# Kernel tuning notes

Measured on AMD Instinct MI355X. Metric: run time of the kernel, lower is better.

## Reference

```python
import jax, jax.numpy as jnp
import numpy as np


def _diag(x, ax1, ax2):
    """Extract diagonal over (ax1, ax2), placing the diag index back at ax1."""
    return jnp.moveaxis(jnp.diagonal(x, axis1=ax1, axis2=ax2), -1, ax1)


def _contractions(x):
    """All mean contractions of a 3rd-order equivariant tensor x: [B,n,n,n,C].
    Returns (a2 [B,n,n,6C], a1 [B,n,10C], a0 [B,5C])."""
    s1 = jnp.mean(x, axis=1)          # [B,n,n,C]
    s2 = jnp.mean(x, axis=2)
    s3 = jnp.mean(x, axis=3)
    d12 = _diag(x, 1, 2)              # x[b,i,i,k,c] -> [B,n,n,C]
    d13 = _diag(x, 1, 3)              # x[b,i,j,i,c]
    d23 = _diag(x, 2, 3)              # x[b,k,i,i,c]
    a2 = jnp.concatenate([s1, s2, s3, d12, d13, d23], axis=-1)  # [B,n,n,6C]

    # first-order: 3 double sums + 6 diag sums + 1 triple diag = 10C
    fo_double = [jnp.mean(x, axis=(1, 2)), jnp.mean(x, axis=(1, 3)),
                 jnp.mean(x, axis=(2, 3))]
    fo_diag = []
    for d in (d12, d13, d23):
        fo_diag.append(jnp.mean(d, axis=1))
        fo_diag.append(jnp.mean(d, axis=2))
    triple_diag = _diag(d23, 1, 2)    # x[b,i,i,i,c] -> [B,n,C]
    a1 = jnp.concatenate(fo_double + fo_diag + [triple_diag], axis=-1)  # [B,n,10C]

    # zeroth-order: triple sum + 3 diag double sums + triple-diag sum = 5C
    z = [jnp.mean(fo_double[0], axis=1)]
    z += [jnp.mean(d, axis=(1, 2)) for d in (d12, d13, d23)]
    z += [jnp.mean(triple_diag, axis=1)]
    a0 = jnp.concatenate(z, axis=-1)  # [B,5C]
    return a2, a1, a0


def _forward(x, W22, b22, W12, b12, W12t, b12t, W02, b02, W11, b11, W01, b01):
    a2, a1, a0 = _contractions(x)
    a2_w_t = jnp.concatenate([a2, jnp.swapaxes(a2, 1, 2)], axis=-1)  # [B,n,n,12C]
    # second-order mix -> [B,n,n,O]
    so = (a2_w_t @ W22 + b22
          + (a1 @ W12 + b12)[:, :, None, :]
          + (a1 @ W12t + b12t)[:, None, :, :]
          + (a0 @ W02 + b02)[:, None, None, :])
    # first-order mix -> [B,n,O], added onto the diagonal
    fo = a1 @ W11 + b11 + (a0 @ W01 + b01)[:, None, :]
    idx = jnp.arange(so.shape[1])
    return so.at[:, idx, idx, :].add(fo)


def setup_inputs() -> dict:
    key = jax.random.key(0)
    B, n, C, O = 8, 64, 32, 32
    ks = jax.random.split(key, 13)

    def w(k, fan_in):
        return (jax.random.normal(k, (fan_in, O), jnp.float32)
                / np.float32(np.sqrt(fan_in)))

    def b(k):
        return jax.random.normal(k, (O,), jnp.float32) * 0.02

    return {
        "x": jax.random.normal(ks[0], (B, n, n, n, C), jnp.float32),
        "W22": w(ks[1], 12 * C), "b22": b(ks[2]),
        "W12": w(ks[3], 10 * C), "b12": b(ks[4]),
        "W12t": w(ks[5], 10 * C), "b12t": b(ks[6]),
        "W02": w(ks[7], 5 * C), "b02": b(ks[8]),
        "W11": w(ks[9], 10 * C), "b11": b(ks[10]),
        "W01": w(ks[11], 5 * C), "b01": b(ks[12]),
    }


def reference(x, W22, b22, W12, b12, W12t, b12t, W02, b02, W11, b11, W01, b01):
    return _forward(x, W22, b22, W12, b12, W12t, b12t, W02, b02, W11, b11, W01, b01)
```

## Files before the change

kernel.cpp:

```cpp
#include <hip/hip_runtime.h>
#include <hip/hip_bf16.h>
#include <stdint.h>

#define NC   2048
#define NNC  131072
#define N3C  8388608
#define CMPE 1048576

typedef unsigned short u16;

__device__ __forceinline__ u16 bf16b(float x){
    unsigned u = __float_as_uint(x);
    u += 0x7FFFu + ((u >> 16) & 1u);
    return (u16)(u >> 16);
}
__device__ __forceinline__ float b2f(u16 h){ return __uint_as_float(((unsigned)h) << 16); }
__device__ __forceinline__ float lo16(unsigned u){ return __uint_as_float(u << 16); }
__device__ __forceinline__ float hi16(unsigned u){ return __uint_as_float(u & 0xFFFF0000u); }
__device__ __forceinline__ void f4acc(float4& a, const float4 b){
    a.x += b.x; a.y += b.y; a.z += b.z; a.w += b.w;
}
__device__ __forceinline__ void addp4(float4& a, const uint2 u){
    a.x += lo16(u.x); a.y += hi16(u.x); a.z += lo16(u.y); a.w += hi16(u.y);
}
__device__ __forceinline__ uint2 pack4(float4 v){
    uint2 r;
    r.x = (unsigned)bf16b(v.x) | ((unsigned)bf16b(v.y) << 16);
    r.y = (unsigned)bf16b(v.z) | ((unsigned)bf16b(v.w) << 16);
    return r;
}
__device__ __forceinline__ uint2 pack4s(float4 v, float s){
    v.x *= s; v.y *= s; v.z *= s; v.w *= s;
    return pack4(v);
}

__global__ __launch_bounds__(256, 4) void k_pass1(
    const float* __restrict__ x,
    u16* __restrict__ p1, u16* __restrict__ p2,
    u16* __restrict__ s3ph, u16* __restrict__ c_d12,
    u16* __restrict__ c_d13, u16* __restrict__ c_d23)
{
    int blk = blockIdx.x;
    int kh = blk & 1, jg = (blk >> 1) & 7, ig = (blk >> 4) & 7, b = blk >> 7;
    int t = threadIdx.x;
    int ktl = t >> 3, kt = kh * 32 + ktl, c4 = (t & 7) * 4;

    __shared__ u16 s3l[8][32][34];

    float4 p1a[8];
    #pragma unroll
    for (int a = 0; a < 8; ++a) p1a[a] = make_float4(0,0,0,0);

    const float* xb = x + (size_t)b * N3C + (size_t)ig * 8 * NNC
                        + (size_t)jg * 8 * NC + (size_t)kh * 1024;

    int rjj = t >> 5, rc = t & 31;

    float4 v[8];
    #pragma unroll
    for (int jj = 0; jj < 8; ++jj)
        v[jj] = *reinterpret_cast<const float4*>(xb + (size_t)jj * NC + 4 * t);

    for (int ii = 0; ii < 8; ++ii){
        int i = ig * 8 + ii;
        float4 q = make_float4(0,0,0,0);
        #pragma unroll
        for (int jj = 0; jj < 8; ++jj){
            int j = jg * 8 + jj;
            f4acc(p1a[jj], v[jj]);
            f4acc(q, v[jj]);
            s3l[jj][c4 + 0][ktl] = bf16b(v[jj].x);
            s3l[jj][c4 + 1][ktl] = bf16b(v[jj].y);
            s3l[jj][c4 + 2][ktl] = bf16b(v[jj].z);
            s3l[jj][c4 + 3][ktl] = bf16b(v[jj].w);
            if (kt == i)
                *reinterpret_cast<uint2*>(c_d13 + (((size_t)(b * 64 + i)) * 64 + j) * 32 + c4) = pack4(v[jj]);
            if (kt == j)
                *reinterpret_cast<uint2*>(c_d23 + (((size_t)(b * 64 + i)) * 64 + j) * 32 + c4) = pack4(v[jj]);
            if (i == j)
                *reinterpret_cast<uint2*>(c_d12 + ((size_t)(b * 64 + i)) * 2048 + kh * 1024 + 4 * (size_t)t) = pack4(v[jj]);
        }
        *reinterpret_cast<uint2*>(p2 + ((size_t)((b * 8 + jg) * 64 + i)) * 2048 + kh * 1024 + 4 * (size_t)t) = pack4(q);

        __syncthreads();
        float4 vn[8];
        if (ii < 7){
            #pragma unroll
            for (int jj = 0; jj < 8; ++jj)
                vn[jj] = *reinterpret_cast<const float4*>(xb + (size_t)(ii + 1) * NNC + (size_t)jj * NC + 4 * t);
        }
        {
            const unsigned* sp = reinterpret_cast<const unsigned*>(&s3l[rjj][rc][0]);
            float s = 0.f;
            #pragma unroll
            for (int g = 0; g < 16; ++g){
                unsigned u = sp[g];
                s += lo16(u) + hi16(u);
            }
            s3ph[(size_t)kh * 1048576 + (((size_t)(b * 64 + i)) * 64 + jg * 8 + rjj) * 32 + rc] = bf16b(s);
        }
        __syncthreads();
        if (ii < 7){
            #pragma unroll
            for (int jj = 0; jj < 8; ++jj) v[jj] = vn[jj];
        }
    }
    #pragma unroll
    for (int jj = 0; jj < 8; ++jj)
        *reinterpret_cast<uint2*>(p1 + ((size_t)((b * 8 + ig) * 64 + jg * 8 + jj)) * 2048 + kh * 1024 + 4 * (size_t)t) = pack4(p1a[jj]);
}

__global__ __launch_bounds__(256) void k_reduce(
    const u16* __restrict__ p1, const u16* __restrict__ p2,
    const u16* __restrict__ s3ph,
    u16* __restrict__ c_s1, u16* __restrict__ c_s2, u16* __restrict__ c_s3)
{
    int blk = blockIdx.x;
    int b = blk / 96, rr = blk % 96, sx = rr >> 5, ch = rr & 31;
    int t = threadIdx.x;
    if (sx == 2){
        #pragma unroll
        for (int r2 = 0; r2 < 2; ++r2){
            int row = ch * 2 + r2;
            #pragma unroll
            for (int e = 0; e < 2; ++e){
                size_t base = ((size_t)(b * 64 + row)) * 2048 + e * 1024 + 4 * t;
                float4 a = make_float4(0,0,0,0);
                addp4(a, *reinterpret_cast<const uint2*>(s3ph + base));
                addp4(a, *reinterpret_cast<const uint2*>(s3ph + 1048576 + base));
                *reinterpret_cast<uint2*>(c_s3 + base) = pack4s(a, 1.f/64.f);
            }
        }
        return;
    }
    const u16* P = sx ? p2 : p1;
    u16* O = sx ? c_s2 : c_s1;
    #pragma unroll
    for (int r2 = 0; r2 < 2; ++r2){
        int row = ch * 2 + r2;
        float4 a0v = make_float4(0,0,0,0), a1v = make_float4(0,0,0,0);
        #pragma unroll
        for (int g = 0; g < 8; ++g){
            const u16* src = P + ((size_t)((b * 8 + g) * 64 + row)) * 2048;
            addp4(a0v, *reinterpret_cast<const uint2*>(src + 4 * t));
            addp4(a1v, *reinterpret_cast<const uint2*>(src + 1024 + 4 * t));
        }
        u16* ob = O + ((size_t)(b * 64 + row)) * 2048;
        *reinterpret_cast<uint2*>(ob + 4 * t)        = pack4s(a0v, 1.f/64.f);
        *reinterpret_cast<uint2*>(ob + 1024 + 4 * t) = pack4s(a1v, 1.f/64.f);
    }
}

__global__ __launch_bounds__(256) void k_a1a0(
    const u16* __restrict__ comps,
    float* __restrict__ a1, float* __restrict__ a0)
{
    int b = blockIdx.x / 5, m = blockIdx.x % 5;
    const int cidx [5] = {0, 1, 3, 4, 5};
    const int rowch[5] = {1, 2, 4, 6, 8};
    const int colch[5] = {0, -1, 3, 5, 7};
    const int a0i  [5] = {0, -1, 1, 2, 3};

    const u16* M = comps + (size_t)cidx[m] * CMPE + (size_t)b * NNC;
    int t = threadIdx.x, c = t & 31, qb = (t >> 5) * 8;
    float colacc[8] = {0,0,0,0,0,0,0,0};
    __shared__ float red[2048];
    __shared__ float rowc[64][32];
    for (int p0 = 0; p0 < 64; p0 += 8){
        #pragma unroll
        for (int pp = 0; pp < 8; ++pp){
            const u16* row = M + (size_t)(p0 + pp) * 2048;
            float part = 0.f;
            #pragma unroll
            for (int kk = 0; kk < 8; ++kk){
                float v = b2f(row[(qb + kk) * 32 + c]);
                colacc[kk] += v; part += v;
            }
            red[pp * 256 + t] = part;
        }
        __syncthreads();
        {
            int pp = t >> 5, cc = t & 31;
            float ssum = 0.f;
            #pragma unroll
            for (int g = 0; g < 8; ++g) ssum += red[pp * 256 + g * 32 + cc];
            rowc[p0 + pp][cc] = ssum;
            a1[((size_t)b * 64 + p0 + pp) * 320 + rowch[m] * 32 + cc] = ssum * (1.f/64.f);
        }
        __syncthreads();
    }
    if (colch[m] >= 0){
        #pragma unroll
        for (int kk = 0; kk < 8; ++kk)
            a1[((size_t)b * 64 + qb + kk) * 320 + colch[m] * 32 + c] = colacc[kk] * (1.f/64.f);
    }
    if (a0i[m] >= 0){
        int pg = t >> 5;
        float tp = 0.f;
        #pragma unroll
        for (int r = 0; r < 8; ++r) tp += rowc[pg * 8 + r][c];
        red[t] = tp;
        __syncthreads();
        if (t < 32){
            float tot = 0.f;
            #pragma unroll
            for (int g = 0; g < 8; ++g) tot += red[g * 32 + t];
            a0[(size_t)b * 160 + a0i[m] * 32 + t] = tot * (1.f/4096.f);
        }
    }
    if (m == 2){
        __syncthreads();
        float dp = 0.f;
        #pragma unroll
        for (int r = 0; r < 8; ++r){
            int p = (t >> 5) + 8 * r;
            float dv = b2f(M[((size_t)p * 64 + p) * 32 + c]);
            a1[((size_t)b * 64 + p) * 320 + 288 + c] = dv;
            dp += dv;
        }
        red[t] = dp;
        __syncthreads();
        if (t < 32){
            float s = 0.f;
            #pragma unroll
            for (int g = 0; g < 8; ++g) s += red[g * 32 + t];
            a0[(size_t)b * 160 + 128 + t] = s * (1.f/64.f);
        }
    }
}

__global__ __launch_bounds__(256) void k_uvec(
    const float* __restrict__ a1, const float* __restrict__ a0,
    float* __restrict__ u1p, float* __restrict__ u1t, float* __restrict__ fov,
    const float* __restrict__ W12,  const float* __restrict__ b12,
    const float* __restrict__ W12t, const float* __restrict__ b12t,
    const float* __restrict__ W02,  const float* __restrict__ b02,
    const float* __restrict__ W11,  const float* __restrict__ b11,
    const float* __restrict__ W01,  const float* __restrict__ b01,
    const float* __restrict__ b22)
{
    int b = blockIdx.x >> 3, pg = blockIdx.x & 7;
    int t = threadIdx.x;
    int p = pg * 8 + (t >> 5), o = t & 31;
    const float* a1r = a1 + ((size_t)b * 64 + p) * 320;
    const float* a0r = a0 + (size_t)b * 160;
    float accP = b12[o] + b02[o] + b22[o];
    float accT = b12t[o];
    float accF = b11[o] + b01[o];
    for (int f = 0; f < 320; ++f){
        float a = a1r[f];
        accP = fmaf(a, W12 [f * 32 + o], accP);
        accT = fmaf(a, W12t[f * 32 + o], accT);
        accF = fmaf(a, W11 [f * 32 + o], accF);
    }
    for (int g = 0; g < 160; ++g){
        float a = a0r[g];
        accP = fmaf(a, W02[g * 32 + o], accP);
        accF = fmaf(a, W01[g * 32 + o], accF);
    }
    size_t idx = ((size_t)b * 64 + p) * 32 + o;
    u1p[idx] = accP; u1t[idx] = accT; fov[idx] = accF;
}

__global__ __launch_bounds__(256, 2) void k_out(
    const u16* __restrict__ comps, const float* __restrict__ W22,
    const float* __restrict__ u1p, const float* __restrict__ u1t,
    const float* __restrict__ fov, float* __restrict__ out)
{
    __shared__ __align__(16) u16 Ast[192 * 68];
    __shared__ __align__(16) u16 Bst[192 * 68];
    __shared__ __align__(16) u16 Wls[192 * 32];
    int blk = blockIdx.x;
    int b = blk >> 6, p = blk & 63;
    int t = threadIdx.x;
    int q = t >> 2, c8 = (t & 3) * 8;

    #pragma unroll
    for (int t6 = 0; t6 < 6; ++t6){
        const u16* cmp = comps + (size_t)t6 * CMPE + (size_t)b * NNC;
        uint4 av = *reinterpret_cast<const uint4*>(cmp + (size_t)p * 2048 + q * 32 + c8);
        uint4 bv = *reinterpret_cast<const uint4*>(cmp + (size_t)q * 2048 + p * 32 + c8);
        int fb = t6 * 32 + c8;
        Ast[(fb+0)*68 + q] = (u16)av.x; Ast[(fb+1)*68 + q] = (u16)(av.x >> 16);
        Ast[(fb+2)*68 + q] = (u16)av.y; Ast[(fb+3)*68 + q] = (u16)(av.y >> 16);
        Ast[(fb+4)*68 + q] = (u16)av.z; Ast[(fb+5)*68 + q] = (u16)(av.z >> 16);
        Ast[(fb+6)*68 + q] = (u16)av.w; Ast[(fb+7)*68 + q] = (u16)(av.w >> 16);
        Bst[(fb+0)*68 + q] = (u16)bv.x; Bst[(fb+1)*68 + q] = (u16)(bv.x >> 16);
        Bst[(fb+2)*68 + q] = (u16)bv.y; Bst[(fb+3)*68 + q] = (u16)(bv.y >> 16);
        Bst[(fb+4)*68 + q] = (u16)bv.z; Bst[(fb+5)*68 + q] = (u16)(bv.z >> 16);
        Bst[(fb+6)*68 + q] = (u16)bv.w; Bst[(fb+7)*68 + q] = (u16)(bv.w >> 16);
    }
    #pragma unroll
    for (int r = 0; r < 6; ++r){
        int idx = t + r * 256;
        int f = idx >> 3, o4 = (idx & 7) * 4;
        float4 w = *reinterpret_cast<const float4*>(W22 + (size_t)idx * 4);
        Wls[f*32 + o4 + 0] = bf16b(w.x); Wls[f*32 + o4 + 1] = bf16b(w.y);
        Wls[f*32 + o4 + 2] = bf16b(w.z); Wls[f*32 + o4 + 3] = bf16b(w.w);
    }
    __syncthreads();

    int qi = t & 15, oi = t >> 4;
    int q0 = qi * 4, o0 = oi * 2;
    float acc00=0,acc01=0,acc10=0,acc11=0,acc20=0,acc21=0,acc30=0,acc31=0;

    #pragma unroll 8
    for (int f = 0; f < 192; ++f){
        uint2 a4 = *reinterpret_cast<const uint2*>(Ast + f * 68 + q0);
        unsigned wp = *reinterpret_cast<const unsigned*>(Wls + f * 32 + o0);
        float w0v = lo16(wp), w1v = hi16(wp);
        float A0v = lo16(a4.x), A1v = hi16(a4.x), A2v = lo16(a4.y), A3v = hi16(a4.y);
        acc00 = fmaf(A0v, w0v, acc00); acc01 = fmaf(A0v, w1v, acc01);
        acc10 = fmaf(A1v, w0v, acc10); acc11 = fmaf(A1v, w1v, acc11);
        acc20 = fmaf(A2v, w0v, acc20); acc21 = fmaf(A2v, w1v, acc21);
        acc30 = fmaf(A3v, w0v, acc30); acc31 = fmaf(A3v, w1v, acc31);
    }
    __syncthreads();
    #pragma unroll
    for (int r = 0; r < 6; ++r){
        int idx = t + r * 256;
        int f = idx >> 3, o4 = (idx & 7) * 4;
        float4 w = *reinterpret_cast<const float4*>(W22 + 6144 + (size_t)idx * 4);
        Wls[f*32 + o4 + 0] = bf16b(w.x); Wls[f*32 + o4 + 1] = bf16b(w.y);
        Wls[f*32 + o4 + 2] = bf16b(w.z); Wls[f*32 + o4 + 3] = bf16b(w.w);
    }
    __syncthreads();
    #pragma unroll 8
    for (int f = 0; f < 192; ++f){
        uint2 a4 = *reinterpret_cast<const uint2*>(Bst + f * 68 + q0);
        unsigned wp = *reinterpret_cast<const unsigned*>(Wls + f * 32 + o0);
        float w0v = lo16(wp), w1v = hi16(wp);
        float A0v = lo16(a4.x), A1v = hi16(a4.x), A2v = lo16(a4.y), A3v = hi16(a4.y);
        acc00 = fmaf(A0v, w0v, acc00); acc01 = fmaf(A0v, w1v, acc01);
        acc10 = fmaf(A1v, w0v, acc10); acc11 = fmaf(A1v, w1v, acc11);
        acc20 = fmaf(A2v, w0v, acc20); acc21 = fmaf(A2v, w1v, acc21);
        acc30 = fmaf(A3v, w0v, acc30); acc31 = fmaf(A3v, w1v, acc31);
    }

    size_t ub = ((size_t)b * 64 + p) * 32;
    float up0 = u1p[ub + o0], up1 = u1p[ub + o0 + 1];
    const float* fovp = fov + ub;
    float accs[4][2] = {{acc00,acc01},{acc10,acc11},{acc20,acc21},{acc30,acc31}};
    #pragma unroll
    for (int iq = 0; iq < 4; ++iq){
        int qq = q0 + iq;
        size_t tb = ((size_t)b * 64 + qq) * 32;
        float e0 = up0 + u1t[tb + o0];
        float e1 = up1 + u1t[tb + o0 + 1];
        if (qq == p){ e0 += fovp[o0]; e1 += fovp[o0 + 1]; }
        float2 v; v.x = accs[iq][0] + e0; v.y = accs[iq][1] + e1;
        *reinterpret_cast<float2*>(out + (((size_t)b * 64 + p) * 64 + qq) * 32 + o0) = v;
    }
}

extern "C" void kernel_launch(void* const* d_in, const int* in_sizes, int n_in,
                              void* d_out, int out_size, void* d_ws, size_t ws_size,
                              hipStream_t stream){
    const float* x    = (const float*)d_in[0];
    const float* W22  = (const float*)d_in[1];
    const float* b22  = (const float*)d_in[2];
    const float* W12  = (const float*)d_in[3];
    const float* b12  = (const float*)d_in[4];
    const float* W12t = (const float*)d_in[5];
    const float* b12t = (const float*)d_in[6];
    const float* W02  = (const float*)d_in[7];
    const float* b02  = (const float*)d_in[8];
    const float* W11  = (const float*)d_in[9];
    const float* b11  = (const float*)d_in[10];
    const float* W01  = (const float*)d_in[11];
    const float* b01  = (const float*)d_in[12];
    float* out = (float*)d_out;
    float* ws  = (float*)d_ws;

    u16*  p1    = (u16*)ws;
    u16*  p2    = (u16*)(ws + 4194304);
    u16*  comps = (u16*)(ws + 8388608);
    u16*  s3ph  = (u16*)(ws + 11534336);
    float* a1   = ws + 12582912;
    float* a0   = ws + 12746752;
    float* u1p  = ws + 12748032;
    float* u1t  = ws + 12764416;
    float* fovv = ws + 12780800;

    k_pass1 <<<1024, 256, 0, stream>>>(x, p1, p2, s3ph,
                comps + 3*(size_t)CMPE, comps + 4*(size_t)CMPE, comps + 5*(size_t)CMPE);
    k_reduce<<<768, 256, 0, stream>>>(p1, p2, s3ph,
                comps, comps + (size_t)CMPE, comps + 2*(size_t)CMPE);
    k_a1a0  <<<40,  256, 0, stream>>>(comps, a1, a0);
    k_uvec  <<<64,  256, 0, stream>>>(a1, a0, u1p, u1t, fovv,
                W12, b12, W12t, b12t, W02, b02, W11, b11, W01, b01, b22);
    k_out   <<<512, 256, 0, stream>>>(comps, W22, u1p, u1t, fovv, out);
}
```

Measured before the change: 129.9 us.

## Use bf16 MFMA for the k_out second-order mix GEMM

Replaces the scalar FMA loop in k_out with 16x16x32 bf16 MFMA instructions. The A and transposed-B components are now stored row-major in a single LDS tile, and W22 is staged transposed into LDS. This removes the per-element transposing LDS scatter and the two-phase weight reload. The output epilogue is remapped to the MFMA accumulator layout, and the weight transpose is now done with scalar strided LDS stores.

Measured after the change: 114.3 us. -12.0%, faster.

```diff
diff --git a/kernel.cpp b/kernel.cpp
--- a/kernel.cpp
+++ b/kernel.cpp
@@ -6,8 +6,11 @@
 #define NNC  131072
 #define N3C  8388608
 #define CMPE 1048576
+#define ASP  392
 
 typedef unsigned short u16;
+typedef short bf16x8 __attribute__((ext_vector_type(8)));
+typedef float f32x4  __attribute__((ext_vector_type(4)));
 
 __device__ __forceinline__ u16 bf16b(float x){
     unsigned u = __float_as_uint(x);
@@ -262,14 +265,13 @@
     u1p[idx] = accP; u1t[idx] = accT; fov[idx] = accF;
 }
 
-__global__ __launch_bounds__(256, 2) void k_out(
+__global__ __launch_bounds__(256) void k_out(
     const u16* __restrict__ comps, const float* __restrict__ W22,
     const float* __restrict__ u1p, const float* __restrict__ u1t,
     const float* __restrict__ fov, float* __restrict__ out)
 {
-    __shared__ __align__(16) u16 Ast[192 * 68];
-    __shared__ __align__(16) u16 Bst[192 * 68];
-    __shared__ __align__(16) u16 Wls[192 * 32];
+    __shared__ __align__(16) u16 As[64 * ASP];
+    __shared__ __align__(16) u16 Wt[32 * ASP];
     int blk = blockIdx.x;
     int b = blk >> 6, p = blk & 63;
     int t = threadIdx.x;
@@ -280,76 +282,45 @@
         const u16* cmp = comps + (size_t)t6 * CMPE + (size_t)b * NNC;
         uint4 av = *reinterpret_cast<const uint4*>(cmp + (size_t)p * 2048 + q * 32 + c8);
         uint4 bv = *reinterpret_cast<const uint4*>(cmp + (size_t)q * 2048 + p * 32 + c8);
-        int fb = t6 * 32 + c8;
-        Ast[(fb+0)*68 + q] = (u16)av.x; Ast[(fb+1)*68 + q] = (u16)(av.x >> 16);
-        Ast[(fb+2)*68 + q] = (u16)av.y; Ast[(fb+3)*68 + q] = (u16)(av.y >> 16);
-        Ast[(fb+4)*68 + q] = (u16)av.z; Ast[(fb+5)*68 + q] = (u16)(av.z >> 16);
-        Ast[(fb+6)*68 + q] = (u16)av.w; Ast[(fb+7)*68 + q] = (u16)(av.w >> 16);
-        Bst[(fb+0)*68 + q] = (u16)bv.x; Bst[(fb+1)*68 + q] = (u16)(bv.x >> 16);
-        Bst[(fb+2)*68 + q] = (u16)bv.y; Bst[(fb+3)*68 + q] = (u16)(bv.y >> 16);
-        Bst[(fb+4)*68 + q] = (u16)bv.z; Bst[(fb+5)*68 + q] = (u16)(bv.z >> 16);
-        Bst[(fb+6)*68 + q] = (u16)bv.w; Bst[(fb+7)*68 + q] = (u16)(bv.w >> 16);
-    }
-    #pragma unroll
-    for (int r = 0; r < 6; ++r){
-        int idx = t + r * 256;
-        int f = idx >> 3, o4 = (idx & 7) * 4;
-        float4 w = *reinterpret_cast<const float4*>(W22 + (size_t)idx * 4);
-        Wls[f*32 + o4 + 0] = bf16b(w.x); Wls[f*32 + o4 + 1] = bf16b(w.y);
-        Wls[f*32 + o4 + 2] = bf16b(w.z); Wls[f*32 + o4 + 3] = bf16b(w.w);
+        *reinterpret_cast<uint4*>(As + q * ASP + t6 * 32 + c8)       = av;
+        *reinterpret_cast<uint4*>(As + q * ASP + 192 + t6 * 32 + c8) = bv;
+    }
+    for (int r = 0; r < 48; ++r){
+        int idx = r * 256 + t;
+        int f = idx >> 5, o = idx & 31;
+        Wt[o * ASP + f] = bf16b(W22[idx]);
     }
     __syncthreads();
 
-    int qi = t & 15, oi = t >> 4;
-    int q0 = qi * 4, o0 = oi * 2;
-    float acc00=0,acc01=0,acc10=0,acc11=0,acc20=0,acc21=0,acc30=0,acc31=0;
-
-    #pragma unroll 8
-    for (int f = 0; f < 192; ++f){
-        uint2 a4 = *reinterpret_cast<const uint2*>(Ast + f * 68 + q0);
-        unsigned wp = *reinterpret_cast<const unsigned*>(Wls + f * 32 + o0);
-        float w0v = lo16(wp), w1v = hi16(wp);
-        float A0v = lo16(a4.x), A1v = hi16(a4.x), A2v = lo16(a4.y), A3v = hi16(a4.y);
-        acc00 = fmaf(A0v, w0v, acc00); acc01 = fmaf(A0v, w1v, acc01);
-        acc10 = fmaf(A1v, w0v, acc10); acc11 = fmaf(A1v, w1v, acc11);
-        acc20 = fmaf(A2v, w0v, acc20); acc21 = fmaf(A2v, w1v, acc21);
-        acc30 = fmaf(A3v, w0v, acc30); acc31 = fmaf(A3v, w1v, acc31);
-    }
-    __syncthreads();
-    #pragma unroll
-    for (int r = 0; r < 6; ++r){
-        int idx = t + r * 256;
-        int f = idx >> 3, o4 = (idx & 7) * 4;
-        float4 w = *reinterpret_cast<const float4*>(W22 + 6144 + (size_t)idx * 4);
-        Wls[f*32 + o4 + 0] = bf16b(w.x); Wls[f*32 + o4 + 1] = bf16b(w.y);
-        Wls[f*32 + o4 + 2] = bf16b(w.z); Wls[f*32 + o4 + 3] = bf16b(w.w);
-    }
-    __syncthreads();
-    #pragma unroll 8
-    for (int f = 0; f < 192; ++f){
-        uint2 a4 = *reinterpret_cast<const uint2*>(Bst + f * 68 + q0);
-        unsigned wp = *reinterpret_cast<const unsigned*>(Wls + f * 32 + o0);
-        float w0v = lo16(wp), w1v = hi16(wp);
-        float A0v = lo16(a4.x), A1v = hi16(a4.x), A2v = lo16(a4.y), A3v = hi16(a4.y);
-        acc00 = fmaf(A0v, w0v, acc00); acc01 = fmaf(A0v, w1v, acc01);
-        acc10 = fmaf(A1v, w0v, acc10); acc11 = fmaf(A1v, w1v, acc11);
-        acc20 = fmaf(A2v, w0v, acc20); acc21 = fmaf(A2v, w1v, acc21);
-        acc30 = fmaf(A3v, w0v, acc30); acc31 = fmaf(A3v, w1v, acc31);
+    int w = t >> 6, lane = t & 63;
+    int l15 = lane & 15, lk = lane >> 4;
+    f32x4 acc0 = {0.f, 0.f, 0.f, 0.f};
+    f32x4 acc1 = {0.f, 0.f, 0.f, 0.f};
+    const u16* arow  = As + (w * 16 + l15) * ASP + lk * 8;
+    const u16* b0row = Wt + l15 * ASP + lk * 8;
+    const u16* b1row = Wt + (16 + l15) * ASP + lk * 8;
+    #pragma unroll
+    for (int ks = 0; ks < 12; ++ks){
+        bf16x8 af  = *reinterpret_cast<const bf16x8*>(arow  + ks * 32);
+        bf16x8 bf0 = *reinterpret_cast<const bf16x8*>(b0row + ks * 32);
+        bf16x8 bf1 = *reinterpret_cast<const bf16x8*>(b1row + ks * 32);
+        acc0 = __builtin_amdgcn_mfma_f32_16x16x32_bf16(af, bf0, acc0, 0, 0, 0);
+        acc1 = __builtin_amdgcn_mfma_f32_16x16x32_bf16(af, bf1, acc1, 0, 0, 0);
     }
 
     size_t ub = ((size_t)b * 64 + p) * 32;
-    float up0 = u1p[ub + o0], up1 = u1p[ub + o0 + 1];
-    const float* fovp = fov + ub;
-    float accs[4][2] = {{acc00,acc01},{acc10,acc11},{acc20,acc21},{acc30,acc31}};
-    #pragma unroll
-    for (int iq = 0; iq < 4; ++iq){
-        int qq = q0 + iq;
+    float up0 = u1p[ub + l15], up1 = u1p[ub + 16 + l15];
+    float fv0 = fov[ub + l15], fv1 = fov[ub + 16 + l15];
+    #pragma unroll
+    for (int r = 0; r < 4; ++r){
+        int qq = w * 16 + lk * 4 + r;
+        size_t ob = (((size_t)b * 64 + p) * 64 + qq) * 32;
         size_t tb = ((size_t)b * 64 + qq) * 32;
-        float e0 = up0 + u1t[tb + o0];
-        float e1 = up1 + u1t[tb + o0 + 1];
-        if (qq == p){ e0 += fovp[o0]; e1 += fovp[o0 + 1]; }
-        float2 v; v.x = accs[iq][0] + e0; v.y = accs[iq][1] + e1;
-        *reinterpret_cast<float2*>(out + (((size_t)b * 64 + p) * 64 + qq) * 32 + o0) = v;
+        float e0 = acc0[r] + up0 + u1t[tb + l15];
+        float e1 = acc1[r] + up1 + u1t[tb + 16 + l15];
+        if (qq == p){ e0 += fv0; e1 += fv1; }
+        out[ob + l15]      = e0;
+        out[ob + 16 + l15] = e1;
     }
 }
 
```
